# Optimization experiments

Measured on AMD Instinct MI355X. Metric: run time of the kernel, lower is better.

The kernel has to match this reference:

```python
import jax, jax.numpy as jnp
import numpy as np

N, K, D = 50000, 32, 128


def setup_inputs() -> dict:
    key = jax.random.key(0)
    k1, k2, k3, k4 = jax.random.split(key, 4)
    v_fea = jax.random.normal(k1, (N, D), dtype=jnp.float32)
    t_emb = jax.random.normal(k2, (N, D), dtype=jnp.float32)
    ef = jax.random.randint(k3, (N, K), 0, N, dtype=jnp.int64)
    # nn.Linear(2D, 2D, bias=False) weight, scaled like torch default init
    W = jax.random.normal(k4, (2 * D, 2 * D), dtype=jnp.float32) * (1.0 / np.sqrt(2 * D))
    return {"v_fea": v_fea, "t_emb": t_emb, "ef": ef, "W": W}


def reference(v_fea, t_emb, ef, W):
    # v: gathered neighbor features [N, K, D]
    v = v_fea[ef]
    # q: [N, 2D]; torch Linear applies x @ W.T
    q = jnp.concatenate([v_fea, t_emb], axis=-1)
    wq = q @ W.T                                   # [N, 2D]
    # k: [N, K, 2D]
    k = jnp.concatenate([v, t_emb[ef]], axis=-1)
    # per-edge score: bmm(k, wq[..., None]) -> [N, K]
    r = jnp.einsum("nkd,nd->nk", k, wq)
    r = jax.nn.softmax(r, axis=1)                  # softmax over neighbors
    # weighted sum over neighbors -> [N, D]
    ef_fea = jnp.einsum("nk,nkd->nd", r, v)
    return ef_fea
```

## Files before the change

kernel.cpp:

```cpp
#include <hip/hip_runtime.h>
#include <hip/hip_bf16.h>

#define D     128
#define TWO_D 256
#define KNB   32

typedef __attribute__((ext_vector_type(8))) short    s8;
typedef __attribute__((ext_vector_type(8))) _Float16 h8;
typedef __attribute__((ext_vector_type(2))) _Float16 h2v;
typedef __attribute__((ext_vector_type(4))) float    f4;

__device__ inline unsigned short f2h(float f) {
    return __builtin_bit_cast(unsigned short, (_Float16)f);
}
__device__ inline float h2f(unsigned short u) {
    return (float)__builtin_bit_cast(_Float16, u);
}

union v16u { s8 s; h2v h[4]; };

__device__ inline float dot8(s8 x, s8 w, float acc) {
#if __has_builtin(__builtin_amdgcn_fdot2)
    v16u ux, uw; ux.s = x; uw.s = w;
#pragma unroll
    for (int j = 0; j < 4; ++j)
        acc = __builtin_amdgcn_fdot2(ux.h[j], uw.h[j], acc, false);
#else
#pragma unroll
    for (int j = 0; j < 8; ++j)
        acc = fmaf(h2f((unsigned short)x[j]), h2f((unsigned short)w[j]), acc);
#endif
    return acc;
}

__global__ __launch_bounds__(256) void cast_kernel(
    const float* __restrict__ a, const float* __restrict__ b,
    unsigned short* __restrict__ ph, int total)
{
    int i = blockIdx.x * 256 + threadIdx.x;
    if (i >= total) return;
    int n = i >> 4, j = i & 15;
    const float4* pv = (const float4*)(a + (size_t)n * D + j * 8);
    const float4* pt = (const float4*)(b + (size_t)n * D + j * 8);
    float4 v0 = pv[0], v1 = pv[1];
    float4 t0 = pt[0], t1 = pt[1];
    s8 qv, qt;
    qv[0]=(short)f2h(v0.x); qv[1]=(short)f2h(v0.y); qv[2]=(short)f2h(v0.z); qv[3]=(short)f2h(v0.w);
    qv[4]=(short)f2h(v1.x); qv[5]=(short)f2h(v1.y); qv[6]=(short)f2h(v1.z); qv[7]=(short)f2h(v1.w);
    qt[0]=(short)f2h(t0.x); qt[1]=(short)f2h(t0.y); qt[2]=(short)f2h(t0.z); qt[3]=(short)f2h(t0.w);
    qt[4]=(short)f2h(t1.x); qt[5]=(short)f2h(t1.y); qt[6]=(short)f2h(t1.z); qt[7]=(short)f2h(t1.w);
    *(s8*)(ph + (size_t)n * TWO_D + j * 8)     = qv;
    *(s8*)(ph + (size_t)n * TWO_D + D + j * 8) = qt;
}

#define BM 128
#define BN 128
#define BK 32
#define LDT 56

__global__ __launch_bounds__(256) void gemm_wq_mfma(
    const unsigned short* __restrict__ ph,
    const float* __restrict__ W, unsigned short* __restrict__ wq_h, int M)
{
    __shared__ unsigned short As[BM][LDT];
    __shared__ unsigned short Bs[BN][LDT];

    const int tid  = threadIdx.x;
    const int w    = tid >> 6;
    const int lane = tid & 63;
    const int quad = lane >> 4;
    const int l16  = lane & 15;
    const int row0 = blockIdx.x * BM;
    const int i0   = blockIdx.y * BN;

    f4 acc[2][8] = {};

    const int srow = tid >> 1;
    const int seg  = tid & 1;
    int ga = row0 + srow; if (ga >= M) ga = M - 1;

    for (int kt = 0; kt < TWO_D; kt += BK) {
        const unsigned short* pa = ph + (size_t)ga * TWO_D + kt + seg * 16;
        s8 a0 = *(const s8*)(pa);
        s8 a1 = *(const s8*)(pa + 8);
        const float* pb = W + (size_t)(i0 + srow) * TWO_D + kt + seg * 16;
        float4 b0 = *(const float4*)(pb);
        float4 b1 = *(const float4*)(pb + 4);
        float4 b2 = *(const float4*)(pb + 8);
        float4 b3 = *(const float4*)(pb + 12);

        __syncthreads();
        *(s8*)&As[srow][seg * 16]     = a0;
        *(s8*)&As[srow][seg * 16 + 8] = a1;
        {
            s8 q0, q1;
            q0[0]=(short)f2h(b0.x); q0[1]=(short)f2h(b0.y); q0[2]=(short)f2h(b0.z); q0[3]=(short)f2h(b0.w);
            q0[4]=(short)f2h(b1.x); q0[5]=(short)f2h(b1.y); q0[6]=(short)f2h(b1.z); q0[7]=(short)f2h(b1.w);
            q1[0]=(short)f2h(b2.x); q1[1]=(short)f2h(b2.y); q1[2]=(short)f2h(b2.z); q1[3]=(short)f2h(b2.w);
            q1[4]=(short)f2h(b3.x); q1[5]=(short)f2h(b3.y); q1[6]=(short)f2h(b3.z); q1[7]=(short)f2h(b3.w);
            *(s8*)&Bs[srow][seg * 16]     = q0;
            *(s8*)&Bs[srow][seg * 16 + 8] = q1;
        }
        __syncthreads();

        s8 af0 = *(const s8*)&As[w * 32 + l16][quad * 8];
        s8 af1 = *(const s8*)&As[w * 32 + 16 + l16][quad * 8];
#pragma unroll
        for (int nt = 0; nt < 8; ++nt) {
            s8 bf = *(const s8*)&Bs[nt * 16 + l16][quad * 8];
            acc[0][nt] = __builtin_amdgcn_mfma_f32_16x16x32_f16(
                __builtin_bit_cast(h8, af0), __builtin_bit_cast(h8, bf), acc[0][nt], 0, 0, 0);
            acc[1][nt] = __builtin_amdgcn_mfma_f32_16x16x32_f16(
                __builtin_bit_cast(h8, af1), __builtin_bit_cast(h8, bf), acc[1][nt], 0, 0, 0);
        }
    }

#pragma unroll
    for (int mt = 0; mt < 2; ++mt) {
#pragma unroll
        for (int nt = 0; nt < 8; ++nt) {
#pragma unroll
            for (int r = 0; r < 4; ++r) {
                int grow = row0 + w * 32 + mt * 16 + quad * 4 + r;
                if (grow < M)
                    wq_h[(size_t)grow * TWO_D + i0 + nt * 16 + l16] = f2h(acc[mt][nt][r]);
            }
        }
    }
}

__global__ __launch_bounds__(256) void attn_kernel(
    const unsigned short* __restrict__ ph, const int* __restrict__ ef,
    const unsigned short* __restrict__ wq_h, float* __restrict__ outp, int M)
{
    const int lane = threadIdx.x & 63;
    const int w    = threadIdx.x >> 6;
    const int n    = blockIdx.x * 4 + w;
    if (n >= M) return;

    const int g = lane >> 4;
    const int j = lane & 15;

    const unsigned short* wp = wq_h + (size_t)n * TWO_D + j * 16;
    s8 wqa = *(const s8*)(wp);
    s8 wqb = *(const s8*)(wp + 8);

    int eidx = 0;
    if (lane < KNB) eidx = ef[n * KNB + lane];

    s8 xa[8], xb[8];
#pragma unroll
    for (int p = 0; p < 8; ++p) {
        int e = __shfl(eidx, 4 * p + g, 64);
        const unsigned short* rp = ph + (size_t)e * TWO_D + j * 16;
        xa[p] = *(const s8*)(rp);
        xb[p] = *(const s8*)(rp + 8);
    }
    __builtin_amdgcn_sched_barrier(0);

    float s[8];
#pragma unroll
    for (int p = 0; p < 8; ++p) {
        float t = dot8(xa[p], wqa, 0.f);
        s[p] = dot8(xb[p], wqb, t);
    }

#pragma unroll
    for (int p = 0; p < 8; ++p) {
#pragma unroll
        for (int off = 8; off; off >>= 1) s[p] += __shfl_xor(s[p], off, 64);
    }
    float m = -1e30f;
#pragma unroll
    for (int p = 0; p < 8; ++p) {
        float sb = __shfl_xor(s[p], 16, 64);
        float m2 = fmaxf(s[p], sb);
        float m3 = __shfl_xor(m2, 32, 64);
        m = fmaxf(m, fmaxf(m2, m3));
    }
    float e[8];
    float psum = 0.f;
#pragma unroll
    for (int p = 0; p < 8; ++p) {
        e[p] = __expf(s[p] - m);
        psum += e[p];
    }
    psum += __shfl_xor(psum, 16, 64);
    psum += __shfl_xor(psum, 32, 64);

    float o[16] = {};
#pragma unroll
    for (int p = 0; p < 8; ++p) {
        v16u ua, ub; ua.s = xa[p]; ub.s = xb[p];
#pragma unroll
        for (int t = 0; t < 4; ++t) {
            o[2*t]     = fmaf(e[p], (float)ua.h[t][0], o[2*t]);
            o[2*t+1]   = fmaf(e[p], (float)ua.h[t][1], o[2*t+1]);
            o[8+2*t]   = fmaf(e[p], (float)ub.h[t][0], o[8+2*t]);
            o[8+2*t+1] = fmaf(e[p], (float)ub.h[t][1], o[8+2*t+1]);
        }
    }
#pragma unroll
    for (int t = 0; t < 16; ++t) {
        o[t] += __shfl_xor(o[t], 16, 64);
        o[t] += __shfl_xor(o[t], 32, 64);
    }

    if (lane < 8) {
        float inv = 1.0f / psum;
        float* orow = outp + (size_t)n * D + lane * 16;
#pragma unroll
        for (int c = 0; c < 4; ++c) {
            float4 st = make_float4(o[4*c] * inv, o[4*c+1] * inv,
                                    o[4*c+2] * inv, o[4*c+3] * inv);
            *(float4*)(orow + 4 * c) = st;
        }
    }
}

extern "C" void kernel_launch(void* const* d_in, const int* in_sizes, int n_in,
                              void* d_out, int out_size, void* d_ws, size_t ws_size,
                              hipStream_t stream)
{
    const float* v_fea = (const float*)d_in[0];
    const float* t_emb = (const float*)d_in[1];
    const int*   ef    = (const int*)d_in[2];
    const float* W     = (const float*)d_in[3];
    float* outp = (float*)d_out;

    const int M = in_sizes[0] / D;
    char* ws = (char*)d_ws;
    unsigned short* wq_h = (unsigned short*)ws;
    unsigned short* ph   = (unsigned short*)(ws + (size_t)M * TWO_D * 2);

    const int total = M * 16;
    cast_kernel<<<(total + 255) / 256, 256, 0, stream>>>(v_fea, t_emb, ph, total);

    dim3 gg((M + BM - 1) / BM, TWO_D / BN);
    gemm_wq_mfma<<<gg, 256, 0, stream>>>(ph, W, wq_h, M);
    attn_kernel<<<(M + 3) / 4, 256, 0, stream>>>(ph, ef, wq_h, outp, M);
}
```

Measured before the change: 226.7 us.

## Use direct global-to-LDS loads in GEMM and attention, with swizzled full-K tiles

```diff
diff --git a/kernel.cpp b/kernel.cpp
--- a/kernel.cpp
+++ b/kernel.cpp
@@ -31,6 +31,19 @@
         acc = fmaf(h2f((unsigned short)x[j]), h2f((unsigned short)w[j]), acc);
 #endif
     return acc;
+}
+
+__device__ inline void gl_lds16(const void* g, void* l) {
+    __builtin_amdgcn_global_load_lds(
+        (const __attribute__((address_space(1))) void*)g,
+        (__attribute__((address_space(3))) void*)l, 16, 0, 0);
+}
+
+__device__ inline s8 pack8(float4 x, float4 y) {
+    s8 q;
+    q[0]=(short)f2h(x.x); q[1]=(short)f2h(x.y); q[2]=(short)f2h(x.z); q[3]=(short)f2h(x.w);
+    q[4]=(short)f2h(y.x); q[5]=(short)f2h(y.y); q[6]=(short)f2h(y.z); q[7]=(short)f2h(y.w);
+    return q;
 }
 
 __global__ __launch_bounds__(256) void cast_kernel(
@@ -44,26 +57,19 @@
     const float4* pt = (const float4*)(b + (size_t)n * D + j * 8);
     float4 v0 = pv[0], v1 = pv[1];
     float4 t0 = pt[0], t1 = pt[1];
-    s8 qv, qt;
-    qv[0]=(short)f2h(v0.x); qv[1]=(short)f2h(v0.y); qv[2]=(short)f2h(v0.z); qv[3]=(short)f2h(v0.w);
-    qv[4]=(short)f2h(v1.x); qv[5]=(short)f2h(v1.y); qv[6]=(short)f2h(v1.z); qv[7]=(short)f2h(v1.w);
-    qt[0]=(short)f2h(t0.x); qt[1]=(short)f2h(t0.y); qt[2]=(short)f2h(t0.z); qt[3]=(short)f2h(t0.w);
-    qt[4]=(short)f2h(t1.x); qt[5]=(short)f2h(t1.y); qt[6]=(short)f2h(t1.z); qt[7]=(short)f2h(t1.w);
-    *(s8*)(ph + (size_t)n * TWO_D + j * 8)     = qv;
-    *(s8*)(ph + (size_t)n * TWO_D + D + j * 8) = qt;
+    *(s8*)(ph + (size_t)n * TWO_D + j * 8)     = pack8(v0, v1);
+    *(s8*)(ph + (size_t)n * TWO_D + D + j * 8) = pack8(t0, t1);
 }
 
 #define BM 128
 #define BN 128
-#define BK 32
-#define LDT 56
 
 __global__ __launch_bounds__(256) void gemm_wq_mfma(
-    const unsigned short* __restrict__ ph,
-    const float* __restrict__ W, unsigned short* __restrict__ wq_h, int M)
-{
-    __shared__ unsigned short As[BM][LDT];
-    __shared__ unsigned short Bs[BN][LDT];
+    const unsigned short* __restrict__ ph, const float* __restrict__ W,
+    unsigned short* __restrict__ wq_h, int M)
+{
+    __shared__ char As[2][128 * 256];
+    __shared__ char Bs[2][128 * 256];
 
     const int tid  = threadIdx.x;
     const int w    = tid >> 6;
@@ -73,47 +79,73 @@
     const int row0 = blockIdx.x * BM;
     const int i0   = blockIdx.y * BN;
 
+    const int srow_off = tid >> 4;
+    const int scol     = (tid & 15) * 16;
+
     f4 acc[2][8] = {};
 
-    const int srow = tid >> 1;
-    const int seg  = tid & 1;
-    int ga = row0 + srow; if (ga >= M) ga = M - 1;
-
-    for (int kt = 0; kt < TWO_D; kt += BK) {
-        const unsigned short* pa = ph + (size_t)ga * TWO_D + kt + seg * 16;
-        s8 a0 = *(const s8*)(pa);
-        s8 a1 = *(const s8*)(pa + 8);
-        const float* pb = W + (size_t)(i0 + srow) * TWO_D + kt + seg * 16;
-        float4 b0 = *(const float4*)(pb);
-        float4 b1 = *(const float4*)(pb + 4);
-        float4 b2 = *(const float4*)(pb + 8);
-        float4 b3 = *(const float4*)(pb + 12);
-
-        __syncthreads();
-        *(s8*)&As[srow][seg * 16]     = a0;
-        *(s8*)&As[srow][seg * 16 + 8] = a1;
-        {
-            s8 q0, q1;
-            q0[0]=(short)f2h(b0.x); q0[1]=(short)f2h(b0.y); q0[2]=(short)f2h(b0.z); q0[3]=(short)f2h(b0.w);
-            q0[4]=(short)f2h(b1.x); q0[5]=(short)f2h(b1.y); q0[6]=(short)f2h(b1.z); q0[7]=(short)f2h(b1.w);
-            q1[0]=(short)f2h(b2.x); q1[1]=(short)f2h(b2.y); q1[2]=(short)f2h(b2.z); q1[3]=(short)f2h(b2.w);
-            q1[4]=(short)f2h(b3.x); q1[5]=(short)f2h(b3.y); q1[6]=(short)f2h(b3.z); q1[7]=(short)f2h(b3.w);
-            *(s8*)&Bs[srow][seg * 16]     = q0;
-            *(s8*)&Bs[srow][seg * 16 + 8] = q1;
-        }
-        __syncthreads();
-
-        s8 af0 = *(const s8*)&As[w * 32 + l16][quad * 8];
-        s8 af1 = *(const s8*)&As[w * 32 + 16 + l16][quad * 8];
-#pragma unroll
-        for (int nt = 0; nt < 8; ++nt) {
-            s8 bf = *(const s8*)&Bs[nt * 16 + l16][quad * 8];
-            acc[0][nt] = __builtin_amdgcn_mfma_f32_16x16x32_f16(
-                __builtin_bit_cast(h8, af0), __builtin_bit_cast(h8, bf), acc[0][nt], 0, 0, 0);
-            acc[1][nt] = __builtin_amdgcn_mfma_f32_16x16x32_f16(
-                __builtin_bit_cast(h8, af1), __builtin_bit_cast(h8, bf), acc[1][nt], 0, 0, 0);
-        }
-    }
+    auto A_dma = [&](int h) {
+#pragma unroll
+        for (int r = 0; r < 8; ++r) {
+            int row = r * 16 + srow_off;
+            int arow = row0 + row; if (arow >= M) arow = M - 1;
+            gl_lds16((const char*)ph + (size_t)arow * 512 + h * 256
+                         + (scol ^ ((row & 7) << 4)),
+                     As[h] + r * 4096 + w * 1024);
+        }
+    };
+    auto compute_half = [&](int h) {
+#pragma unroll
+        for (int kk = 0; kk < 4; ++kk) {
+            int cb = kk * 64 + quad * 16;
+            int ra0 = w * 32 + l16, ra1 = ra0 + 16;
+            s8 af0 = *(const s8*)(As[h] + ra0 * 256 + (cb ^ ((ra0 & 7) << 4)));
+            s8 af1 = *(const s8*)(As[h] + ra1 * 256 + (cb ^ ((ra1 & 7) << 4)));
+#pragma unroll
+            for (int nt = 0; nt < 8; ++nt) {
+                int rb = nt * 16 + l16;
+                s8 bf = *(const s8*)(Bs[h] + rb * 256 + (cb ^ ((rb & 7) << 4)));
+                acc[0][nt] = __builtin_amdgcn_mfma_f32_16x16x32_f16(
+                    __builtin_bit_cast(h8, af0), __builtin_bit_cast(h8, bf), acc[0][nt], 0, 0, 0);
+                acc[1][nt] = __builtin_amdgcn_mfma_f32_16x16x32_f16(
+                    __builtin_bit_cast(h8, af1), __builtin_bit_cast(h8, bf), acc[1][nt], 0, 0, 0);
+            }
+        }
+    };
+
+    A_dma(0);
+    {
+        float4 b0[8][2];
+#pragma unroll
+        for (int r = 0; r < 8; ++r) {
+            int row = r * 16 + srow_off;
+            const float4* src = (const float4*)(W + (size_t)(i0 + row) * TWO_D + (tid & 15) * 8);
+            b0[r][0] = src[0]; b0[r][1] = src[1];
+        }
+#pragma unroll
+        for (int r = 0; r < 8; ++r) {
+            int row = r * 16 + srow_off;
+            *(s8*)(Bs[0] + row * 256 + (scol ^ ((row & 7) << 4))) = pack8(b0[r][0], b0[r][1]);
+        }
+    }
+    __syncthreads();
+
+    A_dma(1);
+    float4 b1[8][2];
+#pragma unroll
+    for (int r = 0; r < 8; ++r) {
+        int row = r * 16 + srow_off;
+        const float4* src = (const float4*)(W + (size_t)(i0 + row) * TWO_D + D + (tid & 15) * 8);
+        b1[r][0] = src[0]; b1[r][1] = src[1];
+    }
+    compute_half(0);
+#pragma unroll
+    for (int r = 0; r < 8; ++r) {
+        int row = r * 16 + srow_off;
+        *(s8*)(Bs[1] + row * 256 + (scol ^ ((row & 7) << 4))) = pack8(b1[r][0], b1[r][1]);
+    }
+    __syncthreads();
+    compute_half(1);
 
 #pragma unroll
     for (int mt = 0; mt < 2; ++mt) {
@@ -129,40 +161,45 @@
     }
 }
 
-__global__ __launch_bounds__(256) void attn_kernel(
+__global__ __launch_bounds__(128) void attn_kernel(
     const unsigned short* __restrict__ ph, const int* __restrict__ ef,
     const unsigned short* __restrict__ wq_h, float* __restrict__ outp, int M)
 {
+    __shared__ char smem[2][16384];
+
     const int lane = threadIdx.x & 63;
     const int w    = threadIdx.x >> 6;
-    const int n    = blockIdx.x * 4 + w;
+    const int n    = blockIdx.x * 2 + w;
     if (n >= M) return;
 
     const int g = lane >> 4;
     const int j = lane & 15;
 
-    const unsigned short* wp = wq_h + (size_t)n * TWO_D + j * 16;
+    const unsigned short* wp = wq_h + (size_t)n * TWO_D + j * 8;
     s8 wqa = *(const s8*)(wp);
-    s8 wqb = *(const s8*)(wp + 8);
+    s8 wqb = *(const s8*)(wp + D);
 
     int eidx = 0;
     if (lane < KNB) eidx = ef[n * KNB + lane];
 
-    s8 xa[8], xb[8];
+    char* base = smem[w];
 #pragma unroll
     for (int p = 0; p < 8; ++p) {
         int e = __shfl(eidx, 4 * p + g, 64);
-        const unsigned short* rp = ph + (size_t)e * TWO_D + j * 16;
-        xa[p] = *(const s8*)(rp);
-        xb[p] = *(const s8*)(rp + 8);
-    }
+        const char* rp = (const char*)ph + (size_t)e * 512 + j * 16;
+        gl_lds16(rp,       base + p * 1024);
+        gl_lds16(rp + 256, base + 8192 + p * 1024);
+    }
+    asm volatile("s_waitcnt vmcnt(0)" ::: "memory");
     __builtin_amdgcn_sched_barrier(0);
 
     float s[8];
 #pragma unroll
     for (int p = 0; p < 8; ++p) {
-        float t = dot8(xa[p], wqa, 0.f);
-        s[p] = dot8(xb[p], wqb, t);
+        s8 v8 = *(const s8*)(base + p * 1024 + lane * 16);
+        s8 t8 = *(const s8*)(base + 8192 + p * 1024 + lane * 16);
+        float t = dot8(v8, wqa, 0.f);
+        s[p] = dot8(t8, wqb, t);
     }
 
 #pragma unroll
@@ -188,33 +225,28 @@
     psum += __shfl_xor(psum, 16, 64);
     psum += __shfl_xor(psum, 32, 64);
 
-    float o[16] = {};
-#pragma unroll
-    for (int p = 0; p < 8; ++p) {
-        v16u ua, ub; ua.s = xa[p]; ub.s = xb[p];
+    float o[8] = {};
+#pragma unroll
+    for (int p = 0; p < 8; ++p) {
+        s8 v8 = *(const s8*)(base + p * 1024 + lane * 16);
+        v16u u; u.s = v8;
 #pragma unroll
         for (int t = 0; t < 4; ++t) {
-            o[2*t]     = fmaf(e[p], (float)ua.h[t][0], o[2*t]);
-            o[2*t+1]   = fmaf(e[p], (float)ua.h[t][1], o[2*t+1]);
-            o[8+2*t]   = fmaf(e[p], (float)ub.h[t][0], o[8+2*t]);
-            o[8+2*t+1] = fmaf(e[p], (float)ub.h[t][1], o[8+2*t+1]);
-        }
-    }
-#pragma unroll
-    for (int t = 0; t < 16; ++t) {
+            o[2*t]   = fmaf(e[p], (float)u.h[t][0], o[2*t]);
+            o[2*t+1] = fmaf(e[p], (float)u.h[t][1], o[2*t+1]);
+        }
+    }
+#pragma unroll
+    for (int t = 0; t < 8; ++t) {
         o[t] += __shfl_xor(o[t], 16, 64);
         o[t] += __shfl_xor(o[t], 32, 64);
     }
 
-    if (lane < 8) {
+    if (lane < 16) {
         float inv = 1.0f / psum;
-        float* orow = outp + (size_t)n * D + lane * 16;
-#pragma unroll
-        for (int c = 0; c < 4; ++c) {
-            float4 st = make_float4(o[4*c] * inv, o[4*c+1] * inv,
-                                    o[4*c+2] * inv, o[4*c+3] * inv);
-            *(float4*)(orow + 4 * c) = st;
-        }
+        float* orow = outp + (size_t)n * D + j * 8;
+        *(float4*)(orow)     = make_float4(o[0]*inv, o[1]*inv, o[2]*inv, o[3]*inv);
+        *(float4*)(orow + 4) = make_float4(o[4]*inv, o[5]*inv, o[6]*inv, o[7]*inv);
     }
 }
 
@@ -238,5 +270,5 @@
 
     dim3 gg((M + BM - 1) / BM, TWO_D / BN);
     gemm_wq_mfma<<<gg, 256, 0, stream>>>(ph, W, wq_h, M);
-    attn_kernel<<<(M + 3) / 4, 256, 0, stream>>>(ph, ef, wq_h, outp, M);
-}
+    attn_kernel<<<(M + 1) / 2, 128, 0, stream>>>(ph, ef, wq_h, outp, M);
+}
```

Result: slower. 240.6 us (+6.1%).
